# Kernel optimization log

Measured on AMD Instinct MI355X. Metric: run time of the kernel, lower is better.

Reference implementation:

```python
import jax, jax.numpy as jnp
import numpy as np

B, N, P = 1, 8192, 2           # batch, volume points, global params
V, K = 5, 8                    # output variables, neighbor samples
H = HA = 256                   # basis hidden, aggregation hidden
DPOS = DGEO = DPAR = 256       # encoding dims
NOISE_INTENSITY = 50.0         # sampling radius = 1/noise_intensity


def setup_inputs() -> dict:
    key = jax.random.key(0)
    ks = jax.random.split(key, 18)
    s = 0.05
    return {
        "volume_mesh_centers": jax.random.normal(ks[0], (B, N, 3), jnp.float32),
        "encoding_g": jax.random.normal(ks[1], (B, N, DGEO), jnp.float32),
        "encoding_node": jax.random.normal(ks[2], (B, N, DPOS), jnp.float32),
        "global_params_values": jax.random.uniform(ks[3], (B, P, 1), jnp.float32, 0.5, 1.5),
        "global_params_reference": jnp.ones((B, P, 1), jnp.float32),
        # per-variable basis MLP (stacked over V)
        "Wb1": s * jax.random.normal(ks[4], (V, 3, H), jnp.float32),
        "bb1": s * jax.random.normal(ks[5], (V, H), jnp.float32),
        "Wb2": s * jax.random.normal(ks[6], (V, H, H), jnp.float32),
        "bb2": s * jax.random.normal(ks[7], (V, H), jnp.float32),
        # parameter model
        "Wp": s * jax.random.normal(ks[8], (P, DPAR), jnp.float32),
        "bp": s * jax.random.normal(ks[9], (DPAR,), jnp.float32),
        # per-variable aggregation MLP; first layer weight split by input block
        "Wa1_basis": s * jax.random.normal(ks[10], (V, H, HA), jnp.float32),
        "Wa1_node": s * jax.random.normal(ks[11], (V, DPOS, HA), jnp.float32),
        "Wa1_geo": s * jax.random.normal(ks[12], (V, DGEO, HA), jnp.float32),
        "Wa1_param": s * jax.random.normal(ks[13], (V, DPAR, HA), jnp.float32),
        "ba1": s * jax.random.normal(ks[14], (V, HA), jnp.float32),
        "Wa2": s * jax.random.normal(ks[15], (V, HA), jnp.float32),
        "ba2": s * jax.random.normal(ks[16], (V,), jnp.float32),
    }


def reference(volume_mesh_centers, encoding_g, encoding_node,
              global_params_values, global_params_reference,
              Wb1, bb1, Wb2, bb2, Wp, bp,
              Wa1_basis, Wa1_node, Wa1_geo, Wa1_param, ba1, Wa2, ba2):
    r = 1.0 / NOISE_INTENSITY
    b, n, _ = volume_mesh_centers.shape
    kd, kr = jax.random.split(jax.random.key(42))

    # sample_sphere: uniform-in-volume samples around each center.
    # NOTE: faithful to torch.rand_like(unsqueezed_center) -> per-coordinate radius.
    d = jax.random.normal(kd, (b, n, K, 3), volume_mesh_centers.dtype)
    d = d / jnp.linalg.norm(d, axis=-1, keepdims=True)
    radii = r * jax.random.uniform(kr, (b, n, K, 3), volume_mesh_centers.dtype) ** (1.0 / 3.0)
    samples = volume_mesh_centers[:, :, None, :] + d * radii
    # perturbed centers: original point first, then K neighbors -> (B,N,S,3)
    coords = jnp.concatenate([volume_mesh_centers[:, :, None, :], samples], axis=2)

    # parameter encoding: normalize by reference, expand over N (value is
    # identical for every point, so compute once per batch), then param MLP.
    ratio = (global_params_values / global_params_reference)[..., 0]  # (B,P)
    pe = jax.nn.relu(ratio @ Wp + bp)  # (B,DPAR)

    # per-variable basis MLP over all perturbed points: (B,N,S,V,H)
    h1 = jax.nn.relu(jnp.einsum('bnsc,vch->bnsvh', coords, Wb1) + bb1)
    h2 = jax.nn.relu(jnp.einsum('bnsvh,vhg->bnsvg', h1, Wb2) + bb2)

    # aggregation layer 1 = Linear(concat(basis, enc_node, enc_g, pe)).
    # Split the concat-matmul; encoding blocks are S-independent -> compute once.
    enc = (jnp.einsum('bnd,vdh->bnvh', encoding_node, Wa1_node)
           + jnp.einsum('bnd,vdh->bnvh', encoding_g, Wa1_geo)
           + jnp.einsum('bd,vdh->bvh', pe, Wa1_param)[:, None]
           + ba1)  # (B,N,V,HA)
    a1 = jax.nn.relu(jnp.einsum('bnsvg,vgh->bnsvh', h2, Wa1_basis) + enc[:, :, None])
    out = jnp.einsum('bnsvh,vh->bnsv', a1, Wa2) + ba2  # (B,N,S,V)

    # average: half weight on center prediction, half on mean of neighbors
    return 0.5 * out[:, :, 0] + 0.5 * jnp.mean(out[:, :, 1:], axis=2)  # (B,N,V)
```

## Files before the change

kernel.cpp:

```cpp
#include <hip/hip_runtime.h>

typedef unsigned int u32;
typedef unsigned short u16;
typedef short short8 __attribute__((ext_vector_type(8)));
typedef float f32x4 __attribute__((ext_vector_type(4)));
typedef u32 u32x2 __attribute__((ext_vector_type(2)));
typedef u32 u32x4 __attribute__((ext_vector_type(4)));

#define DEV static __device__ __forceinline__

__host__ __device__ constexpr u32 rotl32(u32 x, int r){ return (x << r) | (x >> (32 - r)); }
struct TF2 { u32 a, b; };

__host__ __device__ constexpr TF2 threefry2x32(u32 k0, u32 k1, u32 x0, u32 x1){
  u32 ks0 = k0, ks1 = k1, ks2 = k0 ^ k1 ^ 0x1BD11BDAu;
  x0 += ks0; x1 += ks1;
  x0 += x1; x1 = rotl32(x1,13); x1 ^= x0;
  x0 += x1; x1 = rotl32(x1,15); x1 ^= x0;
  x0 += x1; x1 = rotl32(x1,26); x1 ^= x0;
  x0 += x1; x1 = rotl32(x1, 6); x1 ^= x0;
  x0 += ks1; x1 += ks2 + 1u;
  x0 += x1; x1 = rotl32(x1,17); x1 ^= x0;
  x0 += x1; x1 = rotl32(x1,29); x1 ^= x0;
  x0 += x1; x1 = rotl32(x1,16); x1 ^= x0;
  x0 += x1; x1 = rotl32(x1,24); x1 ^= x0;
  x0 += ks2; x1 += ks0 + 2u;
  x0 += x1; x1 = rotl32(x1,13); x1 ^= x0;
  x0 += x1; x1 = rotl32(x1,15); x1 ^= x0;
  x0 += x1; x1 = rotl32(x1,26); x1 ^= x0;
  x0 += x1; x1 = rotl32(x1, 6); x1 ^= x0;
  x0 += ks0; x1 += ks1 + 3u;
  x0 += x1; x1 = rotl32(x1,17); x1 ^= x0;
  x0 += x1; x1 = rotl32(x1,29); x1 ^= x0;
  x0 += x1; x1 = rotl32(x1,16); x1 ^= x0;
  x0 += x1; x1 = rotl32(x1,24); x1 ^= x0;
  x0 += ks1; x1 += ks2 + 4u;
  x0 += x1; x1 = rotl32(x1,13); x1 ^= x0;
  x0 += x1; x1 = rotl32(x1,15); x1 ^= x0;
  x0 += x1; x1 = rotl32(x1,26); x1 ^= x0;
  x0 += x1; x1 = rotl32(x1, 6); x1 ^= x0;
  x0 += ks2; x1 += ks0 + 5u;
  return TF2{x0, x1};
}

DEV u32 rndbits(u32 ka, u32 kb, u32 e){
  TF2 r = threefry2x32(ka, kb, 0u, e);
  return r.a ^ r.b;
}
DEV float u01(u32 bits){
  return __builtin_bit_cast(float, (bits >> 9) | 0x3f800000u) - 1.0f;
}

DEV u32 f2bf(float f){
  u32 x = __builtin_bit_cast(u32, f);
  return (x + 0x7FFFu + ((x >> 16) & 1u)) >> 16;
}
DEV u32 pack2(float lo, float hi){
  u32 r;
  asm("v_cvt_pk_bf16_f32 %0, %1, %2" : "=v"(r) : "v"(lo), "v"(hi));
  return r;
}
DEV float bf2f(u32 h){ return __builtin_bit_cast(float, h << 16); }

DEV int tile32_off(int row, int k){
  return row*64 + ((((k >> 3) ^ ((row >> 1) & 3))) << 4) + ((k & 7) << 1);
}
DEV int act_off(int r, int c){
  return r*512 + ((((c >> 3) ^ (r & 7))) << 4) + ((c & 7) << 1);
}

DEV void gload16(const void* gp, void* lp){
  __builtin_amdgcn_global_load_lds(
      (const __attribute__((address_space(1))) void*)gp,
      (__attribute__((address_space(3))) void*)lp,
      16, 0, 0);
}

DEV f32x4 mfma16(short8 a, short8 b, f32x4 c){
  return __builtin_amdgcn_mfma_f32_16x16x32_bf16(a, b, c, 0, 0, 0);
}

__global__ __launch_bounds__(256) void k_wpre(
    const float* __restrict__ Wb2, const float* __restrict__ Wab,
    const float* __restrict__ Wan, const float* __restrict__ Wag,
    short8* __restrict__ wpre){
  int gid = blockIdx.x*256 + threadIdx.x;
  int v = gid >> 15;
  int rem = gid & 32767;
  short8 pk;
  if(rem < 16384){
    const float* M = (rem < 8192) ? Wb2 : Wab;
    int loc = rem & 8191;
    int kk = loc >> 10;
    int c  = (loc >> 2) & 255;
    int ku = loc & 3;
    int k0 = kk*32 + ku*8;
    #pragma unroll
    for(int j = 0; j < 8; ++j)
      pk[j] = (short)f2bf(M[(v*256 + k0 + j)*256 + c]);
  } else {
    int loc = rem - 16384;
    int kk = loc >> 10;
    int w  = loc & 1023;
    int i  = w >> 8, tt = w & 255;
    int c  = i*64 + (tt >> 2);
    int k0 = kk*32 + (((tt & 3) ^ ((c >> 1) & 3)) << 3);
    #pragma unroll
    for(int j = 0; j < 8; ++j){
      int k = k0 + j;
      float val = (k < 256) ? Wan[(v*256 + k)*256 + c]
                            : Wag[(v*256 + (k - 256))*256 + c];
      pk[j] = (short)f2bf(val);
    }
  }
  wpre[gid] = pk;
}

__global__ __launch_bounds__(256) void k_coords(
    const float* __restrict__ centers, float* __restrict__ coords){
  int q = blockIdx.x*256 + threadIdx.x;
  int n = q >> 3, k = q & 7;
  constexpr TF2 KD = threefry2x32(0u, 42u, 0u, 0u);
  constexpr TF2 KR = threefry2x32(0u, 42u, 0u, 1u);
  float d[3], uu[3];
  #pragma unroll
  for(int c = 0; c < 3; ++c){
    u32 e = (u32)(q*3 + c);
    float fd = u01(rndbits(KD.a, KD.b, e));
    float fr = u01(rndbits(KR.a, KR.b, e));
    float un = fmaxf(-0.99999994f, fd*2.0f + (-0.99999994f));
    d[c]  = 1.41421356f * erfinvf(un);
    uu[c] = fr;
  }
  float nr = sqrtf(d[0]*d[0] + d[1]*d[1] + d[2]*d[2]);
  #pragma unroll
  for(int c = 0; c < 3; ++c){
    float ctr = centers[n*3 + c];
    float val = ctr + (d[c]/nr) * (0.02f * powf(uu[c], 0.33333334f));
    coords[((k + 1)*8192 + n)*3 + c] = val;
    if(k == 0) coords[n*3 + c] = ctr;
  }
}

__global__ __launch_bounds__(256) void k_pecb(
    const float* __restrict__ gpv, const float* __restrict__ gpr,
    const float* __restrict__ Wp,  const float* __restrict__ bp,
    const float* __restrict__ Wap, const float* __restrict__ ba1,
    float* __restrict__ cb){
  __shared__ float pe[256];
  int t = threadIdx.x, v = blockIdx.x;
  float r0 = gpv[0]/gpr[0], r1 = gpv[1]/gpr[1];
  pe[t] = fmaxf(r0*Wp[t] + r1*Wp[256 + t] + bp[t], 0.f);
  __syncthreads();
  float s = ba1[v*256 + t];
  #pragma unroll 8
  for(int d = 0; d < 256; ++d) s += pe[d] * Wap[(v*256 + d)*256 + t];
  cb[v*256 + t] = s;
}

__global__ __launch_bounds__(256) void k_enc(
    const short8* __restrict__ wpre, const float* __restrict__ en,
    const float* __restrict__ eg, const float* __restrict__ cb,
    u16* __restrict__ enc){
  __shared__ __align__(16) char lds[32768];
  char* ach = lds;
  char* bch = lds + 16384;
  int bx0 = blockIdx.x;
  int bx = (bx0 & 7)*80 + (bx0 >> 3);
  int t = threadIdx.x;
  int v  = bx >> 7;
  int n0 = (bx & 127) * 64;
  int wv = t >> 6, lane = t & 63, lc = lane & 15, hi = lane >> 4;
  f32x4 acc[4][4];
  #pragma unroll
  for(int mt = 0; mt < 4; ++mt)
    #pragma unroll
    for(int nt = 0; nt < 4; ++nt) acc[mt][nt] = f32x4{0.f,0.f,0.f,0.f};
  int bsr = t >> 2, bq = t & 3;
  #pragma unroll
  for(int kk = 0; kk < 16; ++kk){
    __syncthreads();
    const short8* wsrc = wpre + (v*32768 + 16384 + kk*1024 + t);
    #pragma unroll
    for(int i = 0; i < 4; ++i) gload16(wsrc + i*256, ach + i*4096 + wv*1024);
    {
      const float* src = ((kk < 8) ? en : eg) + (n0 + bsr)*256 + (kk & 7)*32 + bq*8;
      f32x4 f0 = *(const f32x4*)(src);
      f32x4 f1 = *(const f32x4*)(src + 4);
      u32x4 w; w[0] = pack2(f0[0], f0[1]); w[1] = pack2(f0[2], f0[3]);
      w[2] = pack2(f1[0], f1[1]); w[3] = pack2(f1[2], f1[3]);
      *(u32x4*)(bch + tile32_off(bsr, bq*8)) = w;
    }
    asm volatile("s_waitcnt vmcnt(0)" ::: "memory");
    __syncthreads();
    short8 a[4], b[4];
    #pragma unroll
    for(int mt = 0; mt < 4; ++mt)
      a[mt] = *(const short8*)(ach + tile32_off(64*wv + 16*mt + lc, hi*8));
    #pragma unroll
    for(int nt = 0; nt < 4; ++nt)
      b[nt] = *(const short8*)(bch + tile32_off(16*nt + lc, hi*8));
    #pragma unroll
    for(int mt = 0; mt < 4; ++mt)
      #pragma unroll
      for(int nt = 0; nt < 4; ++nt)
        acc[mt][nt] = mfma16(a[mt], b[nt], acc[mt][nt]);
  }
  __syncthreads();
  #pragma unroll
  for(int mt = 0; mt < 4; ++mt){
    f32x4 cbv = *(const f32x4*)(cb + v*256 + 64*wv + 16*mt + 4*hi);
    #pragma unroll
    for(int nt = 0; nt < 4; ++nt){
      u32x2 pk;
      pk[0] = pack2(acc[mt][nt][0] + cbv[0], acc[mt][nt][1] + cbv[1]);
      pk[1] = pack2(acc[mt][nt][2] + cbv[2], acc[mt][nt][3] + cbv[3]);
      *(u32x2*)(lds + act_off(16*nt + lc, 64*wv + 16*mt + 4*hi)) = pk;
    }
  }
  __syncthreads();
  #pragma unroll
  for(int i = 0; i < 8; ++i){
    int L = i*256 + t; int r = L >> 5; int u = L & 31;
    u32x4 val = *(const u32x4*)(lds + act_off(r, u*8));
    *(u32x4*)(enc + (size_t)(v*8192 + n0 + r)*256 + u*8) = val;
  }
}

__global__ __launch_bounds__(256) void k_main(
    const short8* __restrict__ wpre, const float* __restrict__ coords,
    const float* __restrict__ Wb1, const float* __restrict__ bb1,
    const float* __restrict__ bb2, const u16* __restrict__ enc,
    const float* __restrict__ Wa2, float* __restrict__ part){
  __shared__ __align__(16) char act[32768];
  __shared__ float red[64][4];
  int t = threadIdx.x;
  int bx0 = blockIdx.x;
  int xcd = bx0 & 7;
  int idx = bx0 >> 3;
  int grp = idx / 9;
  int s   = idx - grp*9;
  int g   = xcd*80 + grp;
  int v   = g >> 7;
  int n0  = (g & 127) * 64;
  int wv = t >> 6, lane = t & 63, lc = lane & 15, hi = lane >> 4;

  int base0 = lc*512 + 16*(hi ^ (lc & 3));
  int ks = ((lc >> 2) & 1) * 64;
  const char* bE = act + (base0 + ks);
  const char* bO = act + (base0 - ks);

  f32x4 bv1[4], bv2[4];
  #pragma unroll
  for(int mt = 0; mt < 4; ++mt){
    bv1[mt] = *(const f32x4*)(bb1 + v*256 + 64*wv + 16*mt + 4*hi);
    bv2[mt] = *(const f32x4*)(bb2 + v*256 + 64*wv + 16*mt + 4*hi);
  }

  short8 a1f[4], b1f[4];
  short8 z8 = {};
  #pragma unroll
  for(int i = 0; i < 4; ++i){ a1f[i] = z8; b1f[i] = z8; }
  if(hi == 0){
    #pragma unroll
    for(int mt = 0; mt < 4; ++mt){
      int c = 64*wv + 16*mt + lc;
      float w0 = Wb1[v*768 + c], w1 = Wb1[v*768 + 256 + c], w2 = Wb1[v*768 + 512 + c];
      u32x4 q; q[0] = pack2(w0, w1); q[1] = pack2(w2, w0);
      q[2] = pack2(w1, w2); q[3] = 0u;
      a1f[mt] = __builtin_bit_cast(short8, q);
    }
    #pragma unroll
    for(int nt = 0; nt < 4; ++nt){
      const float* cp = coords + (size_t)(s*8192 + n0 + 16*nt + lc)*3;
      float x = cp[0], y = cp[1], z = cp[2];
      float xh = bf2f(f2bf(x)), yh = bf2f(f2bf(y)), zh = bf2f(f2bf(z));
      u32x4 q;
      q[0] = pack2(x, y);
      q[1] = pack2(z, x - xh);
      q[2] = pack2(y - yh, z - zh);
      q[3] = 0u;
      b1f[nt] = __builtin_bit_cast(short8, q);
    }
  }

  f32x4 acc[4][4];
  #pragma unroll
  for(int mt = 0; mt < 4; ++mt)
    #pragma unroll
    for(int nt = 0; nt < 4; ++nt) acc[mt][nt] = bv1[mt];

  #pragma unroll
  for(int mt = 0; mt < 4; ++mt)
    #pragma unroll
    for(int nt = 0; nt < 4; ++nt)
      acc[mt][nt] = mfma16(a1f[mt], b1f[nt], acc[mt][nt]);

  auto repack = [&](){
    #pragma unroll
    for(int mt = 0; mt < 4; ++mt)
      #pragma unroll
      for(int nt = 0; nt < 4; ++nt){
        f32x4 h = acc[mt][nt];
        u32x2 pk;
        pk[0] = pack2(fmaxf(h[0], 0.f), fmaxf(h[1], 0.f));
        pk[1] = pack2(fmaxf(h[2], 0.f), fmaxf(h[3], 0.f));
        *(u32x2*)(act + act_off(16*nt + lc, 64*wv + 16*mt + 4*hi)) = pk;
      }
  };
  repack();
  #pragma unroll
  for(int mt = 0; mt < 4; ++mt)
    #pragma unroll
    for(int nt = 0; nt < 4; ++nt) acc[mt][nt] = bv2[mt];
  __syncthreads();

  const char* wbytes = (const char*)wpre + (size_t)v*524288 + (size_t)((64*wv + lc)*64 + hi*16);
  auto gemm = [&](int gm){
    const char* pw = wbytes + gm*131072;
    short8 aw[2][4];
    #pragma unroll
    for(int mt = 0; mt < 4; ++mt) aw[0][mt] = *(const short8*)(pw + mt*1024);
    #pragma unroll
    for(int kk = 0; kk < 8; ++kk){
      if(kk < 7){
        #pragma unroll
        for(int mt = 0; mt < 4; ++mt)
          aw[(kk & 1) ^ 1][mt] = *(const short8*)(pw + (kk + 1)*16384 + mt*1024);
      }
      const char* bp = (kk & 1) ? bO : bE;
      short8 bfr[4];
      #pragma unroll
      for(int nt = 0; nt < 4; ++nt)
        bfr[nt] = *(const short8*)(bp + nt*8192 + kk*64);
      #pragma unroll
      for(int mt = 0; mt < 4; ++mt)
        #pragma unroll
        for(int nt = 0; nt < 4; ++nt)
          acc[mt][nt] = mfma16(aw[kk & 1][mt], bfr[nt], acc[mt][nt]);
    }
  };

  gemm(0);
  __syncthreads();
  repack();
  #pragma unroll
  for(int mt = 0; mt < 4; ++mt)
    #pragma unroll
    for(int nt = 0; nt < 4; ++nt) acc[mt][nt] = f32x4{0.f,0.f,0.f,0.f};
  __syncthreads();
  gemm(1);
  __syncthreads();

  {
    const u16* encp = enc + (size_t)(v*8192 + n0)*256;
    #pragma unroll
    for(int i = 0; i < 8; ++i){
      int r = i*8 + (t >> 5); int u = t & 31;
      u32x4 val = *(const u32x4*)(encp + (size_t)r*256 + u*8);
      *(u32x4*)(act + act_off(r, u*8)) = val;
    }
  }
  __syncthreads();

  f32x4 w4[4];
  #pragma unroll
  for(int mt = 0; mt < 4; ++mt)
    w4[mt] = *(const f32x4*)(Wa2 + v*256 + 64*wv + 16*mt + 4*hi);
  #pragma unroll
  for(int nt = 0; nt < 4; ++nt){
    float p = 0.f;
    #pragma unroll
    for(int mt = 0; mt < 4; ++mt){
      u32x2 e2 = *(const u32x2*)(act + act_off(16*nt + lc, 64*wv + 16*mt + 4*hi));
      f32x4 h = acc[mt][nt];
      float a0 = fmaxf(h[0] + bf2f(e2[0] & 0xFFFFu), 0.f);
      float a1 = fmaxf(h[1] + bf2f(e2[0] >> 16),     0.f);
      float a2 = fmaxf(h[2] + bf2f(e2[1] & 0xFFFFu), 0.f);
      float a3 = fmaxf(h[3] + bf2f(e2[1] >> 16),     0.f);
      p += a0*w4[mt][0] + a1*w4[mt][1] + a2*w4[mt][2] + a3*w4[mt][3];
    }
    p += __shfl_xor(p, 16, 64);
    p += __shfl_xor(p, 32, 64);
    if(hi == 0) red[16*nt + lc][wv] = p;
  }
  __syncthreads();
  if(t < 64){
    float sum = red[t][0] + red[t][1] + red[t][2] + red[t][3];
    part[(v*9 + s)*8192 + n0 + t] = sum;
  }
}

__global__ __launch_bounds__(256) void k_fin(
    const float* __restrict__ part, const float* __restrict__ ba2,
    float* __restrict__ out){
  int i = blockIdx.x*256 + threadIdx.x;
  if(i >= 40960) return;
  int n = i / 5, v = i - n*5;
  const float* p = part + v*73728 + n;
  float sm = 0.f;
  #pragma unroll
  for(int s = 1; s < 9; ++s) sm += p[s*8192];
  out[i] = ba2[v] + 0.5f*p[0] + 0.0625f*sm;
}

extern "C" void kernel_launch(void* const* d_in, const int* in_sizes, int n_in,
                              void* d_out, int out_size, void* d_ws, size_t ws_size,
                              hipStream_t stream){
  const float* centers = (const float*)d_in[0];
  const float* eg   = (const float*)d_in[1];
  const float* en   = (const float*)d_in[2];
  const float* gpv  = (const float*)d_in[3];
  const float* gpr  = (const float*)d_in[4];
  const float* Wb1  = (const float*)d_in[5];
  const float* bb1  = (const float*)d_in[6];
  const float* Wb2  = (const float*)d_in[7];
  const float* bb2  = (const float*)d_in[8];
  const float* Wp   = (const float*)d_in[9];
  const float* bp   = (const float*)d_in[10];
  const float* Wab  = (const float*)d_in[11];
  const float* Wan  = (const float*)d_in[12];
  const float* Wag  = (const float*)d_in[13];
  const float* Wap  = (const float*)d_in[14];
  const float* ba1  = (const float*)d_in[15];
  const float* Wa2  = (const float*)d_in[16];
  const float* ba2  = (const float*)d_in[17];
  float* out = (float*)d_out;
  char* ws = (char*)d_ws;

  short8* wpre  = (short8*)(ws);
  float* coords = (float*) (ws + 2621440);
  float* cb     = (float*) (ws + 3506176);
  float* partb  = (float*) (ws + 3511296);
  u16*   enc    = (u16*)   (ws + 4985856);

  k_wpre  <<<640,  256, 0, stream>>>(Wb2, Wab, Wan, Wag, wpre);
  k_coords<<<256,  256, 0, stream>>>(centers, coords);
  k_pecb  <<<5,    256, 0, stream>>>(gpv, gpr, Wp, bp, Wap, ba1, cb);
  k_enc   <<<640,  256, 0, stream>>>(wpre, en, eg, cb, enc);
  k_main  <<<5760, 256, 0, stream>>>(wpre, coords, Wb1, bb1, bb2, enc, Wa2, partb);
  k_fin   <<<160,  256, 0, stream>>>(partb, ba2, out);
}
```

Baseline: 162.9 us.

## Store encoding in MFMA fragment layout and seed second GEMM accumulators

```diff
diff --git a/kernel.cpp b/kernel.cpp
--- a/kernel.cpp
+++ b/kernel.cpp
@@ -61,6 +61,8 @@
   return r;
 }
 DEV float bf2f(u32 h){ return __builtin_bit_cast(float, h << 16); }
+DEV float bflo(u32 w){ return __builtin_bit_cast(float, w << 16); }
+DEV float bfhi(u32 w){ return __builtin_bit_cast(float, w & 0xFFFF0000u); }
 
 DEV int tile32_off(int row, int k){
   return row*64 + ((((k >> 3) ^ ((row >> 1) & 3))) << 4) + ((k & 7) << 1);
@@ -161,7 +163,7 @@
 __global__ __launch_bounds__(256) void k_enc(
     const short8* __restrict__ wpre, const float* __restrict__ en,
     const float* __restrict__ eg, const float* __restrict__ cb,
-    u16* __restrict__ enc){
+    char* __restrict__ encfr){
   __shared__ __align__(16) char lds[32768];
   char* ach = lds;
   char* bch = lds + 16384;
@@ -206,31 +208,28 @@
       for(int nt = 0; nt < 4; ++nt)
         acc[mt][nt] = mfma16(a[mt], b[nt], acc[mt][nt]);
   }
-  __syncthreads();
+  char* encw = encfr + (size_t)bx*32768 + (size_t)t*16;
   #pragma unroll
   for(int mt = 0; mt < 4; ++mt){
     f32x4 cbv = *(const f32x4*)(cb + v*256 + 64*wv + 16*mt + 4*hi);
     #pragma unroll
-    for(int nt = 0; nt < 4; ++nt){
-      u32x2 pk;
-      pk[0] = pack2(acc[mt][nt][0] + cbv[0], acc[mt][nt][1] + cbv[1]);
-      pk[1] = pack2(acc[mt][nt][2] + cbv[2], acc[mt][nt][3] + cbv[3]);
-      *(u32x2*)(lds + act_off(16*nt + lc, 64*wv + 16*mt + 4*hi)) = pk;
-    }
-  }
-  __syncthreads();
-  #pragma unroll
-  for(int i = 0; i < 8; ++i){
-    int L = i*256 + t; int r = L >> 5; int u = L & 31;
-    u32x4 val = *(const u32x4*)(lds + act_off(r, u*8));
-    *(u32x4*)(enc + (size_t)(v*8192 + n0 + r)*256 + u*8) = val;
+    for(int np = 0; np < 2; ++np){
+      u32x4 w;
+      #pragma unroll
+      for(int h = 0; h < 2; ++h){
+        f32x4 a = acc[mt][np*2 + h];
+        w[h*2]     = pack2(a[0] + cbv[0], a[1] + cbv[1]);
+        w[h*2 + 1] = pack2(a[2] + cbv[2], a[3] + cbv[3]);
+      }
+      *(u32x4*)(encw + (mt*2 + np)*4096) = w;
+    }
   }
 }
 
 __global__ __launch_bounds__(256) void k_main(
     const short8* __restrict__ wpre, const float* __restrict__ coords,
     const float* __restrict__ Wb1, const float* __restrict__ bb1,
-    const float* __restrict__ bb2, const u16* __restrict__ enc,
+    const float* __restrict__ bb2, const char* __restrict__ encfr,
     const float* __restrict__ Wa2, float* __restrict__ part){
   __shared__ __align__(16) char act[32768];
   __shared__ float red[64][4];
@@ -285,16 +284,12 @@
   }
 
   f32x4 acc[4][4];
+
   #pragma unroll
   for(int mt = 0; mt < 4; ++mt)
     #pragma unroll
-    for(int nt = 0; nt < 4; ++nt) acc[mt][nt] = bv1[mt];
-
-  #pragma unroll
-  for(int mt = 0; mt < 4; ++mt)
-    #pragma unroll
     for(int nt = 0; nt < 4; ++nt)
-      acc[mt][nt] = mfma16(a1f[mt], b1f[nt], acc[mt][nt]);
+      acc[mt][nt] = mfma16(a1f[mt], b1f[nt], bv1[mt]);
 
   auto repack = [&](){
     #pragma unroll
@@ -309,24 +304,21 @@
       }
   };
   repack();
-  #pragma unroll
-  for(int mt = 0; mt < 4; ++mt)
-    #pragma unroll
-    for(int nt = 0; nt < 4; ++nt) acc[mt][nt] = bv2[mt];
   __syncthreads();
 
-  const char* wbytes = (const char*)wpre + (size_t)v*524288 + (size_t)((64*wv + lc)*64 + hi*16);
-  auto gemm = [&](int gm){
-    const char* pw = wbytes + gm*131072;
+  int loff = (64*wv + lc)*4 + hi;
+  auto gemm = [&](int gm, const f32x4* cinit){
+    const short8* pw0 = wpre + (v*32768 + gm*8192);
     short8 aw[2][4];
     #pragma unroll
-    for(int mt = 0; mt < 4; ++mt) aw[0][mt] = *(const short8*)(pw + mt*1024);
+    for(int mt = 0; mt < 4; ++mt) aw[0][mt] = pw0[loff + mt*64];
     #pragma unroll
     for(int kk = 0; kk < 8; ++kk){
       if(kk < 7){
+        const short8* pwn = wpre + (v*32768 + gm*8192 + (kk + 1)*1024);
         #pragma unroll
         for(int mt = 0; mt < 4; ++mt)
-          aw[(kk & 1) ^ 1][mt] = *(const short8*)(pw + (kk + 1)*16384 + mt*1024);
+          aw[(kk & 1) ^ 1][mt] = pwn[loff + mt*64];
       }
       const char* bp = (kk & 1) ? bO : bE;
       short8 bfr[4];
@@ -336,32 +328,40 @@
       #pragma unroll
       for(int mt = 0; mt < 4; ++mt)
         #pragma unroll
-        for(int nt = 0; nt < 4; ++nt)
-          acc[mt][nt] = mfma16(aw[kk & 1][mt], bfr[nt], acc[mt][nt]);
+        for(int nt = 0; nt < 4; ++nt){
+          f32x4 c = (kk == 0 && cinit) ? cinit[mt] : acc[mt][nt];
+          acc[mt][nt] = mfma16(aw[kk & 1][mt], bfr[nt], c);
+        }
     }
   };
 
-  gemm(0);
+  gemm(0, bv2);
+
+  u32x4 efr[8];
+  {
+    const char* encp = encfr + (size_t)g*32768 + (size_t)t*16;
+    #pragma unroll
+    for(int j = 0; j < 8; ++j)
+      efr[j] = *(const u32x4*)(encp + j*4096);
+  }
+
   __syncthreads();
   repack();
+  __syncthreads();
+
   #pragma unroll
   for(int mt = 0; mt < 4; ++mt)
     #pragma unroll
-    for(int nt = 0; nt < 4; ++nt) acc[mt][nt] = f32x4{0.f,0.f,0.f,0.f};
-  __syncthreads();
-  gemm(1);
-  __syncthreads();
-
-  {
-    const u16* encp = enc + (size_t)(v*8192 + n0)*256;
-    #pragma unroll
-    for(int i = 0; i < 8; ++i){
-      int r = i*8 + (t >> 5); int u = t & 31;
-      u32x4 val = *(const u32x4*)(encp + (size_t)r*256 + u*8);
-      *(u32x4*)(act + act_off(r, u*8)) = val;
-    }
-  }
-  __syncthreads();
+    for(int np = 0; np < 2; ++np){
+      u32x4 w = efr[mt*2 + np];
+      #pragma unroll
+      for(int h = 0; h < 2; ++h){
+        int nt = np*2 + h;
+        acc[mt][nt] = f32x4{bflo(w[h*2]), bfhi(w[h*2]), bflo(w[h*2+1]), bfhi(w[h*2+1])};
+      }
+    }
+
+  gemm(1, nullptr);
 
   f32x4 w4[4];
   #pragma unroll
@@ -372,13 +372,9 @@
     float p = 0.f;
     #pragma unroll
     for(int mt = 0; mt < 4; ++mt){
-      u32x2 e2 = *(const u32x2*)(act + act_off(16*nt + lc, 64*wv + 16*mt + 4*hi));
       f32x4 h = acc[mt][nt];
-      float a0 = fmaxf(h[0] + bf2f(e2[0] & 0xFFFFu), 0.f);
-      float a1 = fmaxf(h[1] + bf2f(e2[0] >> 16),     0.f);
-      float a2 = fmaxf(h[2] + bf2f(e2[1] & 0xFFFFu), 0.f);
-      float a3 = fmaxf(h[3] + bf2f(e2[1] >> 16),     0.f);
-      p += a0*w4[mt][0] + a1*w4[mt][1] + a2*w4[mt][2] + a3*w4[mt][3];
+      p += fmaxf(h[0], 0.f)*w4[mt][0] + fmaxf(h[1], 0.f)*w4[mt][1]
+         + fmaxf(h[2], 0.f)*w4[mt][2] + fmaxf(h[3], 0.f)*w4[mt][3];
     }
     p += __shfl_xor(p, 16, 64);
     p += __shfl_xor(p, 32, 64);
@@ -432,12 +428,12 @@
   float* coords = (float*) (ws + 2621440);
   float* cb     = (float*) (ws + 3506176);
   float* partb  = (float*) (ws + 3511296);
-  u16*   enc    = (u16*)   (ws + 4985856);
+  char*  encfr  = (char*)  (ws + 4985856);
 
   k_wpre  <<<640,  256, 0, stream>>>(Wb2, Wab, Wan, Wag, wpre);
   k_coords<<<256,  256, 0, stream>>>(centers, coords);
   k_pecb  <<<5,    256, 0, stream>>>(gpv, gpr, Wp, bp, Wap, ba1, cb);
-  k_enc   <<<640,  256, 0, stream>>>(wpre, en, eg, cb, enc);
-  k_main  <<<5760, 256, 0, stream>>>(wpre, coords, Wb1, bb1, bb2, enc, Wa2, partb);
+  k_enc   <<<640,  256, 0, stream>>>(wpre, en, eg, cb, encfr);
+  k_main  <<<5760, 256, 0, stream>>>(wpre, coords, Wb1, bb1, bb2, encfr, Wa2, partb);
   k_fin   <<<160,  256, 0, stream>>>(partb, ba2, out);
 }
```

New measurement: 174.7 us. +7.3%, slower.

## Double main-kernel point tile to 128 so each weight fragment feeds twice the MFMAs

Applied to the files above, without the earlier changes.

```diff
diff --git a/kernel.cpp b/kernel.cpp
--- a/kernel.cpp
+++ b/kernel.cpp
@@ -232,17 +232,16 @@
     const float* __restrict__ Wb1, const float* __restrict__ bb1,
     const float* __restrict__ bb2, const u16* __restrict__ enc,
     const float* __restrict__ Wa2, float* __restrict__ part){
-  __shared__ __align__(16) char act[32768];
-  __shared__ float red[64][4];
+  __shared__ __align__(16) char act[65536];
   int t = threadIdx.x;
   int bx0 = blockIdx.x;
   int xcd = bx0 & 7;
   int idx = bx0 >> 3;
   int grp = idx / 9;
   int s   = idx - grp*9;
-  int g   = xcd*80 + grp;
-  int v   = g >> 7;
-  int n0  = (g & 127) * 64;
+  int g   = xcd*40 + grp;
+  int v   = g >> 6;
+  int n0  = (g & 63) * 128;
   int wv = t >> 6, lane = t & 63, lc = lane & 15, hi = lane >> 4;
 
   int base0 = lc*512 + 16*(hi ^ (lc & 3));
@@ -257,10 +256,12 @@
     bv2[mt] = *(const f32x4*)(bb2 + v*256 + 64*wv + 16*mt + 4*hi);
   }
 
-  short8 a1f[4], b1f[4];
+  short8 a1f[4], b1f[8];
   short8 z8 = {};
   #pragma unroll
-  for(int i = 0; i < 4; ++i){ a1f[i] = z8; b1f[i] = z8; }
+  for(int i = 0; i < 4; ++i) a1f[i] = z8;
+  #pragma unroll
+  for(int i = 0; i < 8; ++i) b1f[i] = z8;
   if(hi == 0){
     #pragma unroll
     for(int mt = 0; mt < 4; ++mt){
@@ -271,8 +272,9 @@
       a1f[mt] = __builtin_bit_cast(short8, q);
     }
     #pragma unroll
-    for(int nt = 0; nt < 4; ++nt){
-      const float* cp = coords + (size_t)(s*8192 + n0 + 16*nt + lc)*3;
+    for(int nt = 0; nt < 8; ++nt){
+      int nloc = 64*(nt >> 2) + 16*(nt & 3) + lc;
+      const float* cp = coords + (size_t)(s*8192 + n0 + nloc)*3;
       float x = cp[0], y = cp[1], z = cp[2];
       float xh = bf2f(f2bf(x)), yh = bf2f(f2bf(y)), zh = bf2f(f2bf(z));
       u32x4 q;
@@ -284,35 +286,36 @@
     }
   }
 
-  f32x4 acc[4][4];
-  #pragma unroll
-  for(int mt = 0; mt < 4; ++mt)
-    #pragma unroll
-    for(int nt = 0; nt < 4; ++nt) acc[mt][nt] = bv1[mt];
-
-  #pragma unroll
-  for(int mt = 0; mt < 4; ++mt)
-    #pragma unroll
-    for(int nt = 0; nt < 4; ++nt)
+  f32x4 acc[4][8];
+  #pragma unroll
+  for(int mt = 0; mt < 4; ++mt)
+    #pragma unroll
+    for(int nt = 0; nt < 8; ++nt) acc[mt][nt] = bv1[mt];
+
+  #pragma unroll
+  for(int mt = 0; mt < 4; ++mt)
+    #pragma unroll
+    for(int nt = 0; nt < 8; ++nt)
       acc[mt][nt] = mfma16(a1f[mt], b1f[nt], acc[mt][nt]);
 
   auto repack = [&](){
     #pragma unroll
     for(int mt = 0; mt < 4; ++mt)
       #pragma unroll
-      for(int nt = 0; nt < 4; ++nt){
+      for(int nt = 0; nt < 8; ++nt){
         f32x4 h = acc[mt][nt];
         u32x2 pk;
         pk[0] = pack2(fmaxf(h[0], 0.f), fmaxf(h[1], 0.f));
         pk[1] = pack2(fmaxf(h[2], 0.f), fmaxf(h[3], 0.f));
-        *(u32x2*)(act + act_off(16*nt + lc, 64*wv + 16*mt + 4*hi)) = pk;
+        *(u32x2*)(act + 32768*(nt >> 2)
+                  + act_off(16*(nt & 3) + lc, 64*wv + 16*mt + 4*hi)) = pk;
       }
   };
   repack();
   #pragma unroll
   for(int mt = 0; mt < 4; ++mt)
     #pragma unroll
-    for(int nt = 0; nt < 4; ++nt) acc[mt][nt] = bv2[mt];
+    for(int nt = 0; nt < 8; ++nt) acc[mt][nt] = bv2[mt];
   __syncthreads();
 
   const char* wbytes = (const char*)wpre + (size_t)v*524288 + (size_t)((64*wv + lc)*64 + hi*16);
@@ -329,14 +332,14 @@
           aw[(kk & 1) ^ 1][mt] = *(const short8*)(pw + (kk + 1)*16384 + mt*1024);
       }
       const char* bp = (kk & 1) ? bO : bE;
-      short8 bfr[4];
+      short8 bfr[8];
       #pragma unroll
-      for(int nt = 0; nt < 4; ++nt)
-        bfr[nt] = *(const short8*)(bp + nt*8192 + kk*64);
+      for(int nt = 0; nt < 8; ++nt)
+        bfr[nt] = *(const short8*)(bp + 32768*(nt >> 2) + (nt & 3)*8192 + kk*64);
       #pragma unroll
       for(int mt = 0; mt < 4; ++mt)
         #pragma unroll
-        for(int nt = 0; nt < 4; ++nt)
+        for(int nt = 0; nt < 8; ++nt)
           acc[mt][nt] = mfma16(aw[kk & 1][mt], bfr[nt], acc[mt][nt]);
     }
   };
@@ -347,7 +350,7 @@
   #pragma unroll
   for(int mt = 0; mt < 4; ++mt)
     #pragma unroll
-    for(int nt = 0; nt < 4; ++nt) acc[mt][nt] = f32x4{0.f,0.f,0.f,0.f};
+    for(int nt = 0; nt < 8; ++nt) acc[mt][nt] = f32x4{0.f,0.f,0.f,0.f};
   __syncthreads();
   gemm(1);
   __syncthreads();
@@ -355,10 +358,10 @@
   {
     const u16* encp = enc + (size_t)(v*8192 + n0)*256;
     #pragma unroll
-    for(int i = 0; i < 8; ++i){
-      int r = i*8 + (t >> 5); int u = t & 31;
+    for(int i = 0; i < 16; ++i){
+      int L = i*256 + t; int r = L >> 5; int u = L & 31;
       u32x4 val = *(const u32x4*)(encp + (size_t)r*256 + u*8);
-      *(u32x4*)(act + act_off(r, u*8)) = val;
+      *(u32x4*)(act + 32768*(r >> 6) + act_off(r & 63, u*8)) = val;
     }
   }
   __syncthreads();
@@ -367,12 +370,14 @@
   #pragma unroll
   for(int mt = 0; mt < 4; ++mt)
     w4[mt] = *(const f32x4*)(Wa2 + v*256 + 64*wv + 16*mt + 4*hi);
-  #pragma unroll
-  for(int nt = 0; nt < 4; ++nt){
+  float p4[8];
+  #pragma unroll
+  for(int nt = 0; nt < 8; ++nt){
     float p = 0.f;
     #pragma unroll
     for(int mt = 0; mt < 4; ++mt){
-      u32x2 e2 = *(const u32x2*)(act + act_off(16*nt + lc, 64*wv + 16*mt + 4*hi));
+      u32x2 e2 = *(const u32x2*)(act + 32768*(nt >> 2)
+                    + act_off(16*(nt & 3) + lc, 64*wv + 16*mt + 4*hi));
       f32x4 h = acc[mt][nt];
       float a0 = fmaxf(h[0] + bf2f(e2[0] & 0xFFFFu), 0.f);
       float a1 = fmaxf(h[1] + bf2f(e2[0] >> 16),     0.f);
@@ -382,11 +387,16 @@
     }
     p += __shfl_xor(p, 16, 64);
     p += __shfl_xor(p, 32, 64);
-    if(hi == 0) red[16*nt + lc][wv] = p;
-  }
-  __syncthreads();
-  if(t < 64){
-    float sum = red[t][0] + red[t][1] + red[t][2] + red[t][3];
+    p4[nt] = p;
+  }
+  __syncthreads();
+  float* red = (float*)act;
+  #pragma unroll
+  for(int nt = 0; nt < 8; ++nt)
+    if(hi == 0) red[(64*(nt >> 2) + 16*(nt & 3) + lc)*4 + wv] = p4[nt];
+  __syncthreads();
+  if(t < 128){
+    float sum = red[t*4] + red[t*4 + 1] + red[t*4 + 2] + red[t*4 + 3];
     part[(v*9 + s)*8192 + n0 + t] = sum;
   }
 }
@@ -438,6 +448,6 @@
   k_coords<<<256,  256, 0, stream>>>(centers, coords);
   k_pecb  <<<5,    256, 0, stream>>>(gpv, gpr, Wp, bp, Wap, ba1, cb);
   k_enc   <<<640,  256, 0, stream>>>(wpre, en, eg, cb, enc);
-  k_main  <<<5760, 256, 0, stream>>>(wpre, coords, Wb1, bb1, bb2, enc, Wa2, partb);
+  k_main  <<<2880, 256, 0, stream>>>(wpre, coords, Wb1, bb1, bb2, enc, Wa2, partb);
   k_fin   <<<160,  256, 0, stream>>>(partb, ba2, out);
 }
```

Result: slower. 197.9 us (+21.5%).
